# Optimization experiments

Hardware: AMD Instinct MI355X
Metric: run time of the kernel (lower is better)

The kernel has to match this reference:

```python
import jax, jax.numpy as jnp
import numpy as np

C_IN = 512


def _rms(h, gamma):
    # F.normalize(x, dim=1) * sqrt(C) * gamma  (channel_first, h: [b, c, l])
    c = h.shape[1]
    n = jnp.sqrt(jnp.sum(h * h, axis=1, keepdims=True))
    return h / jnp.maximum(n, 1e-12) * (c ** 0.5) * gamma[None, :, None]


def _pw(w, b, h):
    # 1x1 conv == pointwise linear over channel dim; h: [b, c, l]
    return jnp.einsum('oc,bcl->bol', w, h) + b[None, :, None]


def setup_inputs() -> dict:
    key = jax.random.key(0)
    ks = jax.random.split(key, 10)
    B, C, T, H, W = 1, C_IN, 16, 32, 32
    inp = {'x': jax.random.normal(ks[0], (B, C, T, H, W), jnp.float32)}
    names = ['qs', 'ks', 'vs', 'ps', 'qt', 'kt', 'vt', 'pt']
    for i, n in enumerate(names):
        inp[n + '_w'] = jax.random.normal(ks[i + 1], (C, C), jnp.float32) * 0.02
        inp[n + '_b'] = jnp.zeros((C,), jnp.float32)
    inp['norm_s_gamma'] = jnp.ones((C,), jnp.float32)
    inp['norm_t_gamma'] = jnp.ones((C,), jnp.float32)
    inp['max_temporal_window'] = 8
    return inp


def reference(x, qs_w, qs_b, ks_w, ks_b, vs_w, vs_b, ps_w, ps_b,
              qt_w, qt_b, kt_w, kt_b, vt_w, vt_b, pt_w, pt_b,
              norm_s_gamma, norm_t_gamma, max_temporal_window):
    B, C, T, H, W = x.shape
    scale = C ** -0.5

    # ---- spatial attention: (b t) c (h w) ----
    xs = x.transpose(0, 2, 1, 3, 4).reshape(B * T, C, H * W)
    h = _rms(xs, norm_s_gamma)
    q = _pw(qs_w, qs_b, h)
    k = _pw(ks_w, ks_b, h)
    v = _pw(vs_w, vs_b, h)
    scores = jnp.einsum('bcl,bcm->blm', q, k) * scale  # [bt, HW, HW]
    attn = jax.nn.softmax(scores, axis=-1)
    o = jnp.einsum('bcm,blm->bcl', v, attn)
    xs = xs + _pw(ps_w, ps_b, o)
    x = xs.reshape(B, T, C, H, W).transpose(0, 2, 1, 3, 4)

    # ---- temporal attention: (b h w) c t, causal + bounded window ----
    xt = x.transpose(0, 3, 4, 1, 2).reshape(B * H * W, C, T)
    h = _rms(xt, norm_t_gamma)
    q = _pw(qt_w, qt_b, h)
    k = _pw(kt_w, kt_b, h)
    v = _pw(vt_w, vt_b, h)
    scores = jnp.einsum('bcl,bcm->blm', q, k) * scale  # [bhw, T, T]
    i = jnp.arange(T)[:, None]
    j = jnp.arange(T)[None, :]
    allowed = j <= i  # causal
    if max_temporal_window is not None and max_temporal_window > 0:
        allowed = allowed & (i - j < max_temporal_window)  # sliding window
    mask = jnp.where(allowed, 0.0, jnp.finfo(scores.dtype).min)
    attn = jax.nn.softmax(scores + mask[None], axis=-1)
    o = jnp.einsum('bcm,blm->bcl', v, attn)
    xt = xt + _pw(pt_w, pt_b, o)
    x = xt.reshape(B, H, W, C, T).transpose(0, 3, 4, 1, 2)
    return x
```

## Files before the change

kernel.cpp:

```cpp
#include <hip/hip_runtime.h>

typedef __attribute__((ext_vector_type(8))) short bf16x8;
typedef __attribute__((ext_vector_type(4))) float f32x4;

__device__ __forceinline__ short f2bf(float f) {
  union { float f; unsigned u; } a; a.f = f;
  unsigned r = a.u + 0x7fffu + ((a.u >> 16) & 1u);
  return (short)(r >> 16);
}
__device__ __forceinline__ float bf2f(short s) {
  union { unsigned u; float f; } a;
  a.u = ((unsigned)(unsigned short)s) << 16; return a.f;
}
__device__ __forceinline__ float blo(unsigned u) { union { unsigned u; float f; } a; a.u = u << 16; return a.f; }
__device__ __forceinline__ float bhi(unsigned u) { union { unsigned u; float f; } a; a.u = u & 0xffff0000u; return a.f; }
__device__ __forceinline__ unsigned packbf(float lo, float hi) {
  return (unsigned)(unsigned short)f2bf(lo) | ((unsigned)(unsigned short)f2bf(hi) << 16);
}
__device__ __forceinline__ void ldscp16(const void* g, void* l) {
  __builtin_amdgcn_global_load_lds((const __attribute__((address_space(1))) void*)g,
                                   (__attribute__((address_space(3))) void*)l, 16, 0, 0);
}
__device__ __forceinline__ void stv(float* p, float v) { *p = v; }
__device__ __forceinline__ void stv(short* p, float v) { *p = f2bf(v); }

__global__ __launch_bounds__(256) void zero_f(float* __restrict__ p) {
  p[blockIdx.x * 256 + threadIdx.x] = 0.f;
}

__global__ __launch_bounds__(256) void cvt_w(
    const float* __restrict__ w0, const float* __restrict__ w1,
    const float* __restrict__ w2, const float* __restrict__ w3,
    const float* __restrict__ w4, const float* __restrict__ w5,
    const float* __restrict__ w6, const float* __restrict__ w7,
    const float* __restrict__ g_s, const float* __restrict__ g_t,
    short* __restrict__ out) {
  int idx = blockIdx.x * 256 + threadIdx.x;
  const float* ws[8] = {w0, w1, w2, w3, w4, w5, w6, w7};
  int wi = idx >> 18, c = idx & 511;
  float g = 1.f;
  if (wi <= 2) g = g_s[c];
  else if (wi >= 4 && wi <= 6) g = g_t[c];
  out[idx] = f2bf(ws[wi][idx & 262143] * g);
}

__global__ __launch_bounds__(256) void cvt_b(
    const float* __restrict__ b0, const float* __restrict__ b1,
    const float* __restrict__ b2, const float* __restrict__ b3,
    const float* __restrict__ b4, const float* __restrict__ b5,
    const float* __restrict__ b6, const float* __restrict__ b7,
    float* __restrict__ out) {
  int idx = blockIdx.x * 256 + threadIdx.x;
  const float* bs[8] = {b0, b1, b2, b3, b4, b5, b6, b7};
  out[idx] = bs[idx >> 9][idx & 511];
}

__global__ __launch_bounds__(256) void txp_sumsq(
    const float* __restrict__ src, short* __restrict__ dst,
    float* __restrict__ ss) {
  constexpr long N = 16384;
  __shared__ short T[64][66];
  __shared__ float part[16][16][4];
  const int tid = threadIdx.x;
  const long n0 = (long)blockIdx.x * 64;
  const int c0 = blockIdx.y * 64;
  const int n4 = (tid & 15) * 4;
  float s0 = 0.f, s1 = 0.f, s2 = 0.f, s3 = 0.f;
#pragma unroll
  for (int i = 0; i < 4; ++i) {
    int cl = i * 16 + (tid >> 4);
    float4 v = *(const float4*)&src[(long)(c0 + cl) * N + n0 + n4];
    s0 += v.x * v.x; s1 += v.y * v.y; s2 += v.z * v.z; s3 += v.w * v.w;
    T[n4 + 0][cl] = f2bf(v.x); T[n4 + 1][cl] = f2bf(v.y);
    T[n4 + 2][cl] = f2bf(v.z); T[n4 + 3][cl] = f2bf(v.w);
  }
  part[tid >> 4][tid & 15][0] = s0; part[tid >> 4][tid & 15][1] = s1;
  part[tid >> 4][tid & 15][2] = s2; part[tid >> 4][tid & 15][3] = s3;
  __syncthreads();
  if (tid < 64) {
    float s = 0.f;
#pragma unroll
    for (int cg = 0; cg < 16; ++cg) s += part[cg][tid >> 2][tid & 3];
    atomicAdd(&ss[n0 + tid], s);
  }
#pragma unroll
  for (int p = 0; p < 4; ++p) {
    int nl = p * 16 + (tid >> 4);
    int cl = (tid & 15) * 4;
    uint2 o;
    o.x = (unsigned)(unsigned short)T[nl][cl] |
          ((unsigned)(unsigned short)T[nl][cl + 1] << 16);
    o.y = (unsigned)(unsigned short)T[nl][cl + 2] |
          ((unsigned)(unsigned short)T[nl][cl + 3] << 16);
    *(uint2*)&dst[(n0 + nl) * 512 + c0 + cl] = o;
  }
}

template <typename OutT, int BIAS_MODE, int SCALE_MODE, bool RESID>
__global__ __launch_bounds__(256, 2) void gemm_nt(
    const short* __restrict__ A, const short* __restrict__ B,
    OutT* __restrict__ D, const float* __restrict__ bias,
    const float* __restrict__ ssv, const float* __restrict__ resid,
    int K, int lda, int ldb, int ldd,
    long aBatch, long bBatch, long dBatch, float scale) {
  __shared__ short As[128 * 64];
  __shared__ short Bs[128 * 64];
  const int tid = threadIdx.x;
  const int bz = blockIdx.z;
  const long i0 = (long)blockIdx.x * 128;
  const long j0 = (long)blockIdx.y * 128;
  const short* Ab = A + bz * aBatch + i0 * lda;
  const short* Bb = B + bz * bBatch + j0 * ldb;
  const int srow = tid >> 3, scol = tid & 7;
  const int lane = tid & 63;
  const int wr = ((tid >> 7) & 1) * 64;
  const int wc = ((tid >> 6) & 1) * 64;
  const int quad = lane >> 4, l15 = lane & 15;

  f32x4 acc[4][4] = {};

  for (int k0 = 0; k0 < K; k0 += 64) {
    __syncthreads();
#pragma unroll
    for (int p = 0; p < 4; ++p) {
      int row = p * 32 + srow;
      int gc = (scol ^ (row & 7)) << 3;
      ldscp16(Ab + (long)row * lda + k0 + gc, &As[p * 2048 + tid * 8]);
    }
#pragma unroll
    for (int p = 0; p < 4; ++p) {
      int row = p * 32 + srow;
      int gc = (scol ^ (row & 7)) << 3;
      ldscp16(Bb + (long)row * ldb + k0 + gc, &Bs[p * 2048 + tid * 8]);
    }
    __syncthreads();
#pragma unroll
    for (int kk = 0; kk < 2; ++kk) {
      bf16x8 af[4], bfr[4];
#pragma unroll
      for (int a = 0; a < 4; ++a) {
        int row = wr + a * 16 + l15;
        int g = kk * 4 + quad;
        af[a] = *(const bf16x8*)&As[row * 64 + ((g ^ (row & 7)) << 3)];
      }
#pragma unroll
      for (int b = 0; b < 4; ++b) {
        int row = wc + b * 16 + l15;
        int g = kk * 4 + quad;
        bfr[b] = *(const bf16x8*)&Bs[row * 64 + ((g ^ (row & 7)) << 3)];
      }
#pragma unroll
      for (int a = 0; a < 4; ++a)
#pragma unroll
        for (int b = 0; b < 4; ++b)
          acc[a][b] = __builtin_amdgcn_mfma_f32_16x16x32_bf16(af[a], bfr[b], acc[a][b], 0, 0, 0);
    }
  }

  const long Doff = bz * dBatch;
#pragma unroll
  for (int a = 0; a < 4; ++a) {
    const int rb = (int)i0 + wr + a * 16 + quad * 4;
    float rsc[4];
    if (SCALE_MODE == 1) {
#pragma unroll
      for (int r = 0; r < 4; ++r)
        rsc[r] = 22.627416997969522f / fmaxf(sqrtf(ssv[rb + r]), 1e-12f);
    }
#pragma unroll
    for (int b = 0; b < 4; ++b) {
      const int cc = (int)j0 + wc + b * 16 + l15;
      float csc = 1.f;
      if (SCALE_MODE == 2)
        csc = 22.627416997969522f / fmaxf(sqrtf(ssv[cc]), 1e-12f);
#pragma unroll
      for (int r = 0; r < 4; ++r) {
        float val = acc[a][b][r] * scale;
        if (SCALE_MODE == 1) val *= rsc[r];
        if (SCALE_MODE == 2) val *= csc;
        if (BIAS_MODE == 1) val += bias[rb + r];
        if (BIAS_MODE == 2) val += bias[cc];
        const long off = Doff + (long)(rb + r) * ldd + cc;
        if (RESID) val += resid[off];
        stv(D + off, val);
      }
    }
  }
}

__global__ __launch_bounds__(256) void softmax_rows(short* __restrict__ S) {
  short* p = S + (long)blockIdx.x * 1024;
  const int tid = threadIdx.x;
  uint2 d = ((uint2*)p)[tid];
  float v0 = blo(d.x), v1 = bhi(d.x), v2 = blo(d.y), v3 = bhi(d.y);
  float m = fmaxf(fmaxf(v0, v1), fmaxf(v2, v3));
#pragma unroll
  for (int o = 32; o > 0; o >>= 1) m = fmaxf(m, __shfl_xor(m, o));
  __shared__ float redm[4], reds[4];
  const int wv = tid >> 6;
  if ((tid & 63) == 0) redm[wv] = m;
  __syncthreads();
  m = fmaxf(fmaxf(redm[0], redm[1]), fmaxf(redm[2], redm[3]));
  v0 = __expf(v0 - m); v1 = __expf(v1 - m); v2 = __expf(v2 - m); v3 = __expf(v3 - m);
  float s = v0 + v1 + v2 + v3;
#pragma unroll
  for (int o = 32; o > 0; o >>= 1) s += __shfl_xor(s, o);
  if ((tid & 63) == 0) reds[wv] = s;
  __syncthreads();
  s = reds[0] + reds[1] + reds[2] + reds[3];
  const float inv = 1.f / s;
  d.x = packbf(v0 * inv, v1 * inv);
  d.y = packbf(v2 * inv, v3 * inv);
  ((uint2*)p)[tid] = d;
}

__global__ __launch_bounds__(256) void temporal_attn_v3(
    const short* __restrict__ qkv, const int* __restrict__ wndp,
    short* __restrict__ o, float scale) {
  constexpr int RS = 1032;
  __shared__ short qk[16 * RS];
  __shared__ float Plds[16][17];
  const int tid = threadIdx.x;
  const int w = tid >> 6, lane = tid & 63;
  const int hw = blockIdx.x;
  const int wnd = *wndp;

#pragma unroll
  for (int i = 0; i < 8; ++i) {
    int ci = w * 8 + i;
    int t = ci >> 1, half = ci & 1;
    ldscp16(qkv + (long)(t * 1024 + hw) * 1536 + half * 512 + lane * 8,
            &qk[t * RS + half * 512 + lane * 8]);
  }
  const int c0 = lane * 8;
  uint4 vch[16];
#pragma unroll
  for (int tp = 0; tp < 16; ++tp)
    vch[tp] = *(const uint4*)(qkv + (long)(tp * 1024 + hw) * 1536 + 1024 + c0);
  __syncthreads();

  if (w == 0) {
    const int quad = lane >> 4, m = lane & 15;
    const short* rowp = &qk[m * RS + quad * 8];
    f32x4 sacc = {};
#pragma unroll
    for (int s = 0; s < 16; ++s) {
      bf16x8 aq = *(const bf16x8*)(rowp + s * 32);
      bf16x8 bk = *(const bf16x8*)(rowp + 512 + s * 32);
      sacc = __builtin_amdgcn_mfma_f32_16x16x32_bf16(aq, bk, sacc, 0, 0, 0);
    }
#pragma unroll
    for (int r = 0; r < 4; ++r) {
      const int i = quad * 4 + r;
      const int j = m;
      const bool allowed = (j <= i) && (wnd <= 0 || (i - j) < wnd);
      float val = allowed ? sacc[r] * scale : -1e30f;
      float mx = val;
#pragma unroll
      for (int off = 1; off < 16; off <<= 1) mx = fmaxf(mx, __shfl_xor(mx, off));
      float e = allowed ? __expf(val - mx) : 0.f;
      float sum = e;
#pragma unroll
      for (int off = 1; off < 16; off <<= 1) sum += __shfl_xor(sum, off);
      Plds[i][j] = e / sum;
    }
  }
  __syncthreads();

#pragma unroll
  for (int r = 0; r < 4; ++r) {
    const int t = w * 4 + r;
    const int tlo = (wnd > 0 && t - wnd + 1 > 0) ? t - wnd + 1 : 0;
    float a0 = 0.f, a1 = 0.f, a2 = 0.f, a3 = 0.f,
          a4 = 0.f, a5 = 0.f, a6 = 0.f, a7 = 0.f;
#pragma unroll
    for (int tp = 0; tp < 16; ++tp) {
      const float p = (tp >= tlo && tp <= t) ? Plds[t][tp] : 0.f;
      const uint4 vv = vch[tp];
      a0 += p * blo(vv.x); a1 += p * bhi(vv.x);
      a2 += p * blo(vv.y); a3 += p * bhi(vv.y);
      a4 += p * blo(vv.z); a5 += p * bhi(vv.z);
      a6 += p * blo(vv.w); a7 += p * bhi(vv.w);
    }
    uint4 ov;
    ov.x = packbf(a0, a1); ov.y = packbf(a2, a3);
    ov.z = packbf(a4, a5); ov.w = packbf(a6, a7);
    *(uint4*)(o + (long)(t * 1024 + hw) * 512 + c0) = ov;
  }
}

extern "C" void kernel_launch(void* const* d_in, const int* in_sizes, int n_in,
                              void* d_out, int out_size, void* d_ws, size_t ws_size,
                              hipStream_t stream) {
  const float* x    = (const float*)d_in[0];
  const float* qs_w = (const float*)d_in[1];
  const float* qs_b = (const float*)d_in[2];
  const float* ks_w = (const float*)d_in[3];
  const float* ks_b = (const float*)d_in[4];
  const float* vs_w = (const float*)d_in[5];
  const float* vs_b = (const float*)d_in[6];
  const float* ps_w = (const float*)d_in[7];
  const float* ps_b = (const float*)d_in[8];
  const float* qt_w = (const float*)d_in[9];
  const float* qt_b = (const float*)d_in[10];
  const float* kt_w = (const float*)d_in[11];
  const float* kt_b = (const float*)d_in[12];
  const float* vt_w = (const float*)d_in[13];
  const float* vt_b = (const float*)d_in[14];
  const float* pt_w = (const float*)d_in[15];
  const float* pt_b = (const float*)d_in[16];
  const float* g_s  = (const float*)d_in[17];
  const float* g_t  = (const float*)d_in[18];
  const int*   wnd  = (const int*)d_in[19];
  float* out = (float*)d_out;

  char* w = (char*)d_ws;
  short* Wb   = (short*)(w);
  float* Ball = (float*)(w + (4L << 20));
  float* ss_s = (float*)(w + (4L << 20) + (64 << 10));
  float* ss_t = (float*)(w + (4L << 20) + (128 << 10));
  short* hb   = (short*)(w + (5L << 20));
  short* QK   = (short*)(w + (21L << 20));
  short* vB   = (short*)(w + (53L << 20));
  short* oT   = (short*)(w + (69L << 20));
  short* S    = (short*)(w + (85L << 20));
  (void)in_sizes; (void)n_in; (void)out_size; (void)ws_size;

  const float scale = 0.04419417382415922f;

  zero_f<<<128, 256, 0, stream>>>(ss_s);
  cvt_w<<<8192, 256, 0, stream>>>(qs_w, ks_w, vs_w, ps_w, qt_w, kt_w, vt_w, pt_w,
                                  g_s, g_t, Wb);
  cvt_b<<<16, 256, 0, stream>>>(qs_b, ks_b, vs_b, ps_b, qt_b, kt_b, vt_b, pt_b, Ball);

  txp_sumsq<<<dim3(256, 8, 1), 256, 0, stream>>>(x, hb, ss_s);
  gemm_nt<short, 2, 1, false><<<dim3(128, 8, 1), 256, 0, stream>>>(
      hb, Wb, QK, Ball, ss_s, nullptr, 512, 512, 512, 1024, 0, 0, 0, 1.f);
  gemm_nt<short, 1, 2, false><<<dim3(4, 128, 1), 256, 0, stream>>>(
      Wb + 2 * 262144, hb, vB, Ball + 1024, ss_s, nullptr, 512, 512, 512, 16384,
      0, 0, 0, 1.f);
  gemm_nt<short, 0, 0, false><<<dim3(8, 8, 16), 256, 0, stream>>>(
      QK, QK + 512, S, nullptr, nullptr, nullptr, 512, 1024, 1024, 1024,
      1024L * 1024, 1024L * 1024, 1024L * 1024, scale);
  softmax_rows<<<16384, 256, 0, stream>>>(S);
  gemm_nt<short, 0, 0, false><<<dim3(8, 4, 16), 256, 0, stream>>>(
      S, vB, oT, nullptr, nullptr, nullptr, 1024, 1024, 16384, 512,
      1024L * 1024, 1024L, 1024L * 512, 1.f);
  gemm_nt<float, 1, 0, true><<<dim3(4, 128, 1), 256, 0, stream>>>(
      Wb + 3 * 262144, oT, out, Ball + 1536, nullptr, x, 512, 512, 512, 16384,
      0, 0, 0, 1.f);

  txp_sumsq<<<dim3(256, 8, 1), 256, 0, stream>>>(out, hb, ss_t);
  gemm_nt<short, 2, 1, false><<<dim3(128, 12, 1), 256, 0, stream>>>(
      hb, Wb + 4 * 262144, QK, Ball + 2048, ss_t, nullptr, 512, 512, 512, 1536,
      0, 0, 0, 1.f);
  temporal_attn_v3<<<1024, 256, 0, stream>>>(QK, wnd, oT, scale);
  gemm_nt<float, 1, 0, true><<<dim3(4, 128, 1), 256, 0, stream>>>(
      Wb + 7 * 262144, oT, out, Ball + 3584, nullptr, out, 512, 512, 512, 16384,
      0, 0, 0, 1.f);
}
```

Before: 346.9 us.

## Fuse softmax exp into score GEMM and defer normalization to PV GEMM

Removes the separate softmax_rows pass. The score GEMM epilogue now applies exp directly without subtracting a row max, and accumulates per-row sums with atomics into a new workspace buffer. The PV GEMM then divides each output row by its sum. This saves a full read and write of the 16x1024x1024 bf16 score matrix, but it drops max-subtraction, so large scores could overflow. It also raises launch_bounds occupancy from 2 to 3 blocks per CU, which may increase register pressure.

```diff
diff --git a/kernel.cpp b/kernel.cpp
--- a/kernel.cpp
+++ b/kernel.cpp
@@ -96,13 +96,14 @@
   }
 }
 
-template <typename OutT, int BIAS_MODE, int SCALE_MODE, bool RESID>
-__global__ __launch_bounds__(256, 2) void gemm_nt(
+template <typename OutT, int BIAS_MODE, int SCALE_MODE, bool RESID, bool EXP>
+__global__ __launch_bounds__(256, 3) void gemm_nt(
     const short* __restrict__ A, const short* __restrict__ B,
     OutT* __restrict__ D, const float* __restrict__ bias,
-    const float* __restrict__ ssv, const float* __restrict__ resid,
+    const float* __restrict__ ssv, float* __restrict__ rs,
+    const float* __restrict__ resid,
     int K, int lda, int ldb, int ldd,
-    long aBatch, long bBatch, long dBatch, float scale) {
+    long aBatch, long bBatch, long dBatch, long sBatch, float scale) {
   __shared__ short As[128 * 64];
   __shared__ short Bs[128 * 64];
   const int tid = threadIdx.x;
@@ -167,6 +168,12 @@
       for (int r = 0; r < 4; ++r)
         rsc[r] = 22.627416997969522f / fmaxf(sqrtf(ssv[rb + r]), 1e-12f);
     }
+    if (SCALE_MODE == 3) {
+#pragma unroll
+      for (int r = 0; r < 4; ++r)
+        rsc[r] = 1.f / ssv[bz * sBatch + rb + r];
+    }
+    float rowpart[4] = {0.f, 0.f, 0.f, 0.f};
 #pragma unroll
     for (int b = 0; b < 4; ++b) {
       const int cc = (int)j0 + wc + b * 16 + l15;
@@ -176,7 +183,8 @@
 #pragma unroll
       for (int r = 0; r < 4; ++r) {
         float val = acc[a][b][r] * scale;
-        if (SCALE_MODE == 1) val *= rsc[r];
+        if (EXP) { val = __expf(val); rowpart[r] += val; }
+        if (SCALE_MODE == 1 || SCALE_MODE == 3) val *= rsc[r];
         if (SCALE_MODE == 2) val *= csc;
         if (BIAS_MODE == 1) val += bias[rb + r];
         if (BIAS_MODE == 2) val += bias[cc];
@@ -185,33 +193,16 @@
         stv(D + off, val);
       }
     }
-  }
-}
-
-__global__ __launch_bounds__(256) void softmax_rows(short* __restrict__ S) {
-  short* p = S + (long)blockIdx.x * 1024;
-  const int tid = threadIdx.x;
-  uint2 d = ((uint2*)p)[tid];
-  float v0 = blo(d.x), v1 = bhi(d.x), v2 = blo(d.y), v3 = bhi(d.y);
-  float m = fmaxf(fmaxf(v0, v1), fmaxf(v2, v3));
-#pragma unroll
-  for (int o = 32; o > 0; o >>= 1) m = fmaxf(m, __shfl_xor(m, o));
-  __shared__ float redm[4], reds[4];
-  const int wv = tid >> 6;
-  if ((tid & 63) == 0) redm[wv] = m;
-  __syncthreads();
-  m = fmaxf(fmaxf(redm[0], redm[1]), fmaxf(redm[2], redm[3]));
-  v0 = __expf(v0 - m); v1 = __expf(v1 - m); v2 = __expf(v2 - m); v3 = __expf(v3 - m);
-  float s = v0 + v1 + v2 + v3;
-#pragma unroll
-  for (int o = 32; o > 0; o >>= 1) s += __shfl_xor(s, o);
-  if ((tid & 63) == 0) reds[wv] = s;
-  __syncthreads();
-  s = reds[0] + reds[1] + reds[2] + reds[3];
-  const float inv = 1.f / s;
-  d.x = packbf(v0 * inv, v1 * inv);
-  d.y = packbf(v2 * inv, v3 * inv);
-  ((uint2*)p)[tid] = d;
+    if (EXP) {
+#pragma unroll
+      for (int r = 0; r < 4; ++r) {
+        float s = rowpart[r];
+#pragma unroll
+        for (int off = 1; off < 16; off <<= 1) s += __shfl_xor(s, off);
+        if (l15 == 0) atomicAdd(&rs[bz * sBatch + rb + r], s);
+      }
+    }
+  }
 }
 
 __global__ __launch_bounds__(256) void temporal_attn_v3(
@@ -319,6 +310,7 @@
   float* Ball = (float*)(w + (4L << 20));
   float* ss_s = (float*)(w + (4L << 20) + (64 << 10));
   float* ss_t = (float*)(w + (4L << 20) + (128 << 10));
+  float* rsum = (float*)(w + (4L << 20) + (192 << 10));
   short* hb   = (short*)(w + (5L << 20));
   short* QK   = (short*)(w + (21L << 20));
   short* vB   = (short*)(w + (53L << 20));
@@ -328,34 +320,34 @@
 
   const float scale = 0.04419417382415922f;
 
-  zero_f<<<128, 256, 0, stream>>>(ss_s);
+  zero_f<<<192, 256, 0, stream>>>(ss_s);
   cvt_w<<<8192, 256, 0, stream>>>(qs_w, ks_w, vs_w, ps_w, qt_w, kt_w, vt_w, pt_w,
                                   g_s, g_t, Wb);
   cvt_b<<<16, 256, 0, stream>>>(qs_b, ks_b, vs_b, ps_b, qt_b, kt_b, vt_b, pt_b, Ball);
 
   txp_sumsq<<<dim3(256, 8, 1), 256, 0, stream>>>(x, hb, ss_s);
-  gemm_nt<short, 2, 1, false><<<dim3(128, 8, 1), 256, 0, stream>>>(
-      hb, Wb, QK, Ball, ss_s, nullptr, 512, 512, 512, 1024, 0, 0, 0, 1.f);
-  gemm_nt<short, 1, 2, false><<<dim3(4, 128, 1), 256, 0, stream>>>(
-      Wb + 2 * 262144, hb, vB, Ball + 1024, ss_s, nullptr, 512, 512, 512, 16384,
-      0, 0, 0, 1.f);
-  gemm_nt<short, 0, 0, false><<<dim3(8, 8, 16), 256, 0, stream>>>(
-      QK, QK + 512, S, nullptr, nullptr, nullptr, 512, 1024, 1024, 1024,
-      1024L * 1024, 1024L * 1024, 1024L * 1024, scale);
-  softmax_rows<<<16384, 256, 0, stream>>>(S);
-  gemm_nt<short, 0, 0, false><<<dim3(8, 4, 16), 256, 0, stream>>>(
-      S, vB, oT, nullptr, nullptr, nullptr, 1024, 1024, 16384, 512,
-      1024L * 1024, 1024L, 1024L * 512, 1.f);
-  gemm_nt<float, 1, 0, true><<<dim3(4, 128, 1), 256, 0, stream>>>(
-      Wb + 3 * 262144, oT, out, Ball + 1536, nullptr, x, 512, 512, 512, 16384,
-      0, 0, 0, 1.f);
+  gemm_nt<short, 2, 1, false, false><<<dim3(128, 8, 1), 256, 0, stream>>>(
+      hb, Wb, QK, Ball, ss_s, nullptr, nullptr, 512, 512, 512, 1024,
+      0, 0, 0, 0, 1.f);
+  gemm_nt<short, 1, 2, false, false><<<dim3(4, 128, 1), 256, 0, stream>>>(
+      Wb + 2 * 262144, hb, vB, Ball + 1024, ss_s, nullptr, nullptr,
+      512, 512, 512, 16384, 0, 0, 0, 0, 1.f);
+  gemm_nt<short, 0, 0, false, true><<<dim3(8, 8, 16), 256, 0, stream>>>(
+      QK, QK + 512, S, nullptr, nullptr, rsum, nullptr, 512, 1024, 1024, 1024,
+      1024L * 1024, 1024L * 1024, 1024L * 1024, 1024, scale);
+  gemm_nt<short, 0, 3, false, false><<<dim3(8, 4, 16), 256, 0, stream>>>(
+      S, vB, oT, nullptr, rsum, nullptr, nullptr, 1024, 1024, 16384, 512,
+      1024L * 1024, 1024L, 1024L * 512, 1024, 1.f);
+  gemm_nt<float, 1, 0, true, false><<<dim3(4, 128, 1), 256, 0, stream>>>(
+      Wb + 3 * 262144, oT, out, Ball + 1536, nullptr, nullptr, x,
+      512, 512, 512, 16384, 0, 0, 0, 0, 1.f);
 
   txp_sumsq<<<dim3(256, 8, 1), 256, 0, stream>>>(out, hb, ss_t);
-  gemm_nt<short, 2, 1, false><<<dim3(128, 12, 1), 256, 0, stream>>>(
-      hb, Wb + 4 * 262144, QK, Ball + 2048, ss_t, nullptr, 512, 512, 512, 1536,
-      0, 0, 0, 1.f);
+  gemm_nt<short, 2, 1, false, false><<<dim3(128, 12, 1), 256, 0, stream>>>(
+      hb, Wb + 4 * 262144, QK, Ball + 2048, ss_t, nullptr, nullptr,
+      512, 512, 512, 1536, 0, 0, 0, 0, 1.f);
   temporal_attn_v3<<<1024, 256, 0, stream>>>(QK, wnd, oT, scale);
-  gemm_nt<float, 1, 0, true><<<dim3(4, 128, 1), 256, 0, stream>>>(
-      Wb + 7 * 262144, oT, out, Ball + 3584, nullptr, out, 512, 512, 512, 16384,
-      0, 0, 0, 1.f);
-}
+  gemm_nt<float, 1, 0, true, false><<<dim3(4, 128, 1), 256, 0, stream>>>(
+      Wb + 7 * 262144, oT, out, Ball + 3584, nullptr, nullptr, out,
+      512, 512, 512, 16384, 0, 0, 0, 0, 1.f);
+}
```

After: 332.9 us. 4.0% less time.

## Fuse spatial attention scores, softmax and PV into a flash-style kernel

Applied to the files above, without the earlier changes.

Replaces the three-step spatial attention (a batched QK^T GEMM writing a full bf16 score matrix, a row softmax pass, then a PV GEMM) with one flash_spatial kernel. Each wave keeps its 16 query rows in registers, streams 32-key tiles of K and V through LDS, exponentiates scores, accumulates row sums and does the PV MFMAs into register accumulators. This removes the round trips of the 1024x1024-per-frame score matrix through global memory and two kernel launches. The softmax skips max subtraction, which relies on small score magnitudes and risks overflow for general inputs. The GEMM launch bound also rises to 3 blocks per SM, which may constrain registers; the new kernel uses large register tiles, has only 256 blocks, and does not overlap its tile loads with compute.

```diff
diff --git a/kernel.cpp b/kernel.cpp
--- a/kernel.cpp
+++ b/kernel.cpp
@@ -97,7 +97,7 @@
 }
 
 template <typename OutT, int BIAS_MODE, int SCALE_MODE, bool RESID>
-__global__ __launch_bounds__(256, 2) void gemm_nt(
+__global__ __launch_bounds__(256, 3) void gemm_nt(
     const short* __restrict__ A, const short* __restrict__ B,
     OutT* __restrict__ D, const float* __restrict__ bias,
     const float* __restrict__ ssv, const float* __restrict__ resid,
@@ -188,30 +188,86 @@
   }
 }
 
-__global__ __launch_bounds__(256) void softmax_rows(short* __restrict__ S) {
-  short* p = S + (long)blockIdx.x * 1024;
+__global__ __launch_bounds__(256, 2) void flash_spatial(
+    const short* __restrict__ QK, const short* __restrict__ vB,
+    short* __restrict__ oT, float scale) {
+  __shared__ short Ks[32 * 512];
+  __shared__ short Vs[512 * 40];
+  __shared__ short Plds[4 * 16 * 40];
   const int tid = threadIdx.x;
-  uint2 d = ((uint2*)p)[tid];
-  float v0 = blo(d.x), v1 = bhi(d.x), v2 = blo(d.y), v3 = bhi(d.y);
-  float m = fmaxf(fmaxf(v0, v1), fmaxf(v2, v3));
-#pragma unroll
-  for (int o = 32; o > 0; o >>= 1) m = fmaxf(m, __shfl_xor(m, o));
-  __shared__ float redm[4], reds[4];
-  const int wv = tid >> 6;
-  if ((tid & 63) == 0) redm[wv] = m;
-  __syncthreads();
-  m = fmaxf(fmaxf(redm[0], redm[1]), fmaxf(redm[2], redm[3]));
-  v0 = __expf(v0 - m); v1 = __expf(v1 - m); v2 = __expf(v2 - m); v3 = __expf(v3 - m);
-  float s = v0 + v1 + v2 + v3;
-#pragma unroll
-  for (int o = 32; o > 0; o >>= 1) s += __shfl_xor(s, o);
-  if ((tid & 63) == 0) reds[wv] = s;
-  __syncthreads();
-  s = reds[0] + reds[1] + reds[2] + reds[3];
-  const float inv = 1.f / s;
-  d.x = packbf(v0 * inv, v1 * inv);
-  d.y = packbf(v2 * inv, v3 * inv);
-  ((uint2*)p)[tid] = d;
+  const int w = tid >> 6, lane = tid & 63;
+  const int quad = lane >> 4, l15 = lane & 15;
+  const long tb = (long)blockIdx.y * 1024;
+  const long nbase = tb + blockIdx.x * 64;
+  const int lw = w * 16;
+
+  bf16x8 qf[16];
+  {
+    const short* qrow = QK + (nbase + lw + l15) * 1024 + quad * 8;
+#pragma unroll
+    for (int s = 0; s < 16; ++s) qf[s] = *(const bf16x8*)(qrow + s * 32);
+  }
+  f32x4 oacc[32];
+#pragma unroll
+  for (int cb = 0; cb < 32; ++cb) oacc[cb] = (f32x4){0.f, 0.f, 0.f, 0.f};
+  float lrun[4] = {0.f, 0.f, 0.f, 0.f};
+
+  for (int tile = 0; tile < 32; ++tile) {
+    const int m0 = tile * 32;
+    __syncthreads();
+#pragma unroll
+    for (int i = 0; i < 8; ++i) {
+      int m = w * 8 + i;
+      ldscp16(QK + (tb + m0 + m) * 1024 + 512 + ((lane ^ (m & 7)) << 3),
+              &Ks[m * 512 + lane * 8]);
+    }
+#pragma unroll
+    for (int it = 0; it < 8; ++it) {
+      int idx = it * 256 + tid;
+      int c = idx >> 2, ch = idx & 3;
+      *(uint4*)&Vs[c * 40 + ch * 8] =
+          *(const uint4*)(vB + (long)c * 16384 + tb + m0 + ch * 8);
+    }
+    __syncthreads();
+
+    f32x4 sa0 = {}, sa1 = {};
+#pragma unroll
+    for (int s = 0; s < 16; ++s) {
+      const int slot = ((s * 4 + quad) ^ (l15 & 7)) << 3;
+      bf16x8 b0 = *(const bf16x8*)&Ks[l15 * 512 + slot];
+      bf16x8 b1 = *(const bf16x8*)&Ks[(16 + l15) * 512 + slot];
+      sa0 = __builtin_amdgcn_mfma_f32_16x16x32_bf16(qf[s], b0, sa0, 0, 0, 0);
+      sa1 = __builtin_amdgcn_mfma_f32_16x16x32_bf16(qf[s], b1, sa1, 0, 0, 0);
+    }
+
+#pragma unroll
+    for (int r = 0; r < 4; ++r) {
+      float p0 = __expf(sa0[r] * scale);
+      float p1 = __expf(sa1[r] * scale);
+      float rs = p0 + p1;
+#pragma unroll
+      for (int off = 1; off < 16; off <<= 1) rs += __shfl_xor(rs, off);
+      lrun[r] += rs;
+      Plds[(w * 16 + quad * 4 + r) * 40 + l15] = f2bf(p0);
+      Plds[(w * 16 + quad * 4 + r) * 40 + 16 + l15] = f2bf(p1);
+    }
+    bf16x8 pa = *(const bf16x8*)&Plds[(w * 16 + l15) * 40 + quad * 8];
+#pragma unroll
+    for (int cb = 0; cb < 32; ++cb) {
+      bf16x8 vb = *(const bf16x8*)&Vs[(cb * 16 + l15) * 40 + quad * 8];
+      oacc[cb] = __builtin_amdgcn_mfma_f32_16x16x32_bf16(pa, vb, oacc[cb], 0, 0, 0);
+    }
+  }
+
+  float inv[4];
+#pragma unroll
+  for (int r = 0; r < 4; ++r) inv[r] = 1.f / lrun[r];
+#pragma unroll
+  for (int cb = 0; cb < 32; ++cb)
+#pragma unroll
+    for (int r = 0; r < 4; ++r)
+      oT[(nbase + lw + quad * 4 + r) * 512 + cb * 16 + l15] =
+          f2bf(oacc[cb][r] * inv[r]);
 }
 
 __global__ __launch_bounds__(256) void temporal_attn_v3(
@@ -323,7 +379,6 @@
   short* QK   = (short*)(w + (21L << 20));
   short* vB   = (short*)(w + (53L << 20));
   short* oT   = (short*)(w + (69L << 20));
-  short* S    = (short*)(w + (85L << 20));
   (void)in_sizes; (void)n_in; (void)out_size; (void)ws_size;
 
   const float scale = 0.04419417382415922f;
@@ -337,25 +392,19 @@
   gemm_nt<short, 2, 1, false><<<dim3(128, 8, 1), 256, 0, stream>>>(
       hb, Wb, QK, Ball, ss_s, nullptr, 512, 512, 512, 1024, 0, 0, 0, 1.f);
   gemm_nt<short, 1, 2, false><<<dim3(4, 128, 1), 256, 0, stream>>>(
-      Wb + 2 * 262144, hb, vB, Ball + 1024, ss_s, nullptr, 512, 512, 512, 16384,
-      0, 0, 0, 1.f);
-  gemm_nt<short, 0, 0, false><<<dim3(8, 8, 16), 256, 0, stream>>>(
-      QK, QK + 512, S, nullptr, nullptr, nullptr, 512, 1024, 1024, 1024,
-      1024L * 1024, 1024L * 1024, 1024L * 1024, scale);
-  softmax_rows<<<16384, 256, 0, stream>>>(S);
-  gemm_nt<short, 0, 0, false><<<dim3(8, 4, 16), 256, 0, stream>>>(
-      S, vB, oT, nullptr, nullptr, nullptr, 1024, 1024, 16384, 512,
-      1024L * 1024, 1024L, 1024L * 512, 1.f);
+      Wb + 2 * 262144, hb, vB, Ball + 1024, ss_s, nullptr,
+      512, 512, 512, 16384, 0, 0, 0, 1.f);
+  flash_spatial<<<dim3(16, 16, 1), 256, 0, stream>>>(QK, vB, oT, scale);
   gemm_nt<float, 1, 0, true><<<dim3(4, 128, 1), 256, 0, stream>>>(
-      Wb + 3 * 262144, oT, out, Ball + 1536, nullptr, x, 512, 512, 512, 16384,
-      0, 0, 0, 1.f);
+      Wb + 3 * 262144, oT, out, Ball + 1536, nullptr, x,
+      512, 512, 512, 16384, 0, 0, 0, 1.f);
 
   txp_sumsq<<<dim3(256, 8, 1), 256, 0, stream>>>(out, hb, ss_t);
   gemm_nt<short, 2, 1, false><<<dim3(128, 12, 1), 256, 0, stream>>>(
-      hb, Wb + 4 * 262144, QK, Ball + 2048, ss_t, nullptr, 512, 512, 512, 1536,
-      0, 0, 0, 1.f);
+      hb, Wb + 4 * 262144, QK, Ball + 2048, ss_t, nullptr,
+      512, 512, 512, 1536, 0, 0, 0, 1.f);
   temporal_attn_v3<<<1024, 256, 0, stream>>>(QK, wnd, oT, scale);
   gemm_nt<float, 1, 0, true><<<dim3(4, 128, 1), 256, 0, stream>>>(
-      Wb + 7 * 262144, oT, out, Ball + 3584, nullptr, out, 512, 512, 512, 16384,
-      0, 0, 0, 1.f);
-}
+      Wb + 7 * 262144, oT, out, Ball + 3584, nullptr, out,
+      512, 512, 512, 16384, 0, 0, 0, 1.f);
+}
```

Result: slower. 486.5 us (+40.2%).
